# Performance work log

Hardware: AMD Instinct MI355X
Metric: run time of the kernel (lower is better)

## Reference

```python
import jax, jax.numpy as jnp
import numpy as np

B, C, T = 32, 256, 4096

def setup_inputs() -> dict:
    key = jax.random.key(0)
    k1, k2 = jax.random.split(key)
    x = jax.random.normal(k1, (B, C, T), dtype=jnp.float32)
    gamma = jax.random.normal(k2, (1,), dtype=jnp.float32)
    return {"x": x, "gamma": gamma}

def reference(x, gamma):
    # energy[b,i,j] = <x[b,i,:], x[b,j,:]>  -> (B, C, C)
    energy = jnp.einsum('bit,bjt->bij', x, x)
    # max-subtract trick: softmax over (rowmax - energy)
    energy_new = jnp.max(energy, axis=-1, keepdims=True) - energy
    attention = jax.nn.softmax(energy_new, axis=-1)
    # out[b,i,t] = sum_j attention[b,i,j] * x[b,j,t]
    out = jnp.einsum('bij,bjt->bit', attention, x)
    return gamma * out + x
```

## Files before the change

### kernel.cpp

```cpp
#include <hip/hip_runtime.h>
#include <hip/hip_bf16.h>

#define BATCH 32
#define CDIM  256
#define TDIM  4096

using short8  = __attribute__((ext_vector_type(8))) short;
using floatx4 = __attribute__((ext_vector_type(4))) float;
typedef unsigned short u16;

__device__ __forceinline__ unsigned f2bf(float f) {
  unsigned u = __float_as_uint(f);
  return (u + 0x7fffu + ((u >> 16) & 1u)) >> 16;
}
__device__ __forceinline__ unsigned cvt_pk_bf16(float a, float b) {
  return f2bf(a) | (f2bf(b) << 16);
}
__device__ __forceinline__ float bf_lo(unsigned u) { return __uint_as_float(u << 16); }
__device__ __forceinline__ float bf_hi(unsigned u) { return __uint_as_float(u & 0xffff0000u); }

__device__ __forceinline__ void glds16(const void* g, void* l) {
  __builtin_amdgcn_global_load_lds(
      (const __attribute__((address_space(1))) void*)g,
      (__attribute__((address_space(3))) void*)l, 16, 0, 0);
}

__global__ __launch_bounds__(256)
void split_t_kernel(const float* __restrict__ x, u16* __restrict__ hx,
                    u16* __restrict__ lx, u16* __restrict__ hxT) {
  __shared__ u16 ht[64][72];

  const int bx  = blockIdx.x;
  const int b   = bx >> 8;
  const int j0  = ((bx >> 6) & 3) << 6;
  const int t0  = (bx & 63) << 6;
  const int tid = threadIdx.x;
  const int jr  = tid >> 2;
  const int tc  = (tid & 3) << 4;

  const size_t xoff = ((size_t)b << 20) + (size_t)(j0 + jr) * TDIM + t0 + tc;
  const float4 a0 = ((const float4*)(x + xoff))[0];
  const float4 a1 = ((const float4*)(x + xoff))[1];
  const float4 a2 = ((const float4*)(x + xoff))[2];
  const float4 a3 = ((const float4*)(x + xoff))[3];
  const float4 aa[4] = {a0, a1, a2, a3};

  unsigned h[8], l[8];
#pragma unroll
  for (int u = 0; u < 4; ++u) {
    h[2 * u]     = cvt_pk_bf16(aa[u].x, aa[u].y);
    h[2 * u + 1] = cvt_pk_bf16(aa[u].z, aa[u].w);
    l[2 * u]     = cvt_pk_bf16(aa[u].x - bf_lo(h[2 * u]),     aa[u].y - bf_hi(h[2 * u]));
    l[2 * u + 1] = cvt_pk_bf16(aa[u].z - bf_lo(h[2 * u + 1]), aa[u].w - bf_hi(h[2 * u + 1]));
  }

  u16* ph = hx + xoff;
  *(uint4*)ph       = make_uint4(h[0], h[1], h[2], h[3]);
  *(uint4*)(ph + 8) = make_uint4(h[4], h[5], h[6], h[7]);
  u16* pl = lx + xoff;
  *(uint4*)pl       = make_uint4(l[0], l[1], l[2], l[3]);
  *(uint4*)(pl + 8) = make_uint4(l[4], l[5], l[6], l[7]);

#pragma unroll
  for (int u = 0; u < 16; ++u)
    ht[tc + u][jr] = (u16)((u & 1) ? (h[u >> 1] >> 16) : (h[u >> 1] & 0xffffu));
  __syncthreads();

  const int tr = tid >> 2;
  const int jc = (tid & 3) << 4;
  u16* pt = hxT + ((size_t)b << 20) + (size_t)(t0 + tr) * CDIM + j0 + jc;
  *(uint4*)pt       = *(const uint4*)&ht[tr][jc];
  *(uint4*)(pt + 8) = *(const uint4*)&ht[tr][jc + 8];
}

__global__ __launch_bounds__(256)
void split_kernel(const float* __restrict__ x, u16* __restrict__ hx,
                  u16* __restrict__ lx) {
  const unsigned gid0 = blockIdx.x * 256 + threadIdx.x;
#pragma unroll
  for (int it = 0; it < 8; ++it) {
    const size_t g8 = ((size_t)gid0 + (size_t)it * (2048u * 256u)) * 8;
    const float4 a = *(const float4*)(x + g8);
    const float4 c = *(const float4*)(x + g8 + 4);
    unsigned h0 = cvt_pk_bf16(a.x, a.y), h1 = cvt_pk_bf16(a.z, a.w);
    unsigned h2 = cvt_pk_bf16(c.x, c.y), h3 = cvt_pk_bf16(c.z, c.w);
    unsigned l0 = cvt_pk_bf16(a.x - bf_lo(h0), a.y - bf_hi(h0));
    unsigned l1 = cvt_pk_bf16(a.z - bf_lo(h1), a.w - bf_hi(h1));
    unsigned l2 = cvt_pk_bf16(c.x - bf_lo(h2), c.y - bf_hi(h2));
    unsigned l3 = cvt_pk_bf16(c.z - bf_lo(h3), c.w - bf_hi(h3));
    *(uint4*)(hx + g8) = make_uint4(h0, h1, h2, h3);
    *(uint4*)(lx + g8) = make_uint4(l0, l1, l2, l3);
  }
}

__global__ __launch_bounds__(512, 1)
void gram_gemm(const u16* __restrict__ hx, const u16* __restrict__ lx,
               float* __restrict__ S, float* __restrict__ E2) {
  __shared__ __align__(16) short lds[2 * 20480];

  const int tid = threadIdx.x;
  const int bx  = blockIdx.x;

  const int s8  = bx & 7;
  const int seq = bx >> 3;
  const int b   = s8 + ((seq >> 3) << 3);
  const int job = seq & 7;
  const int i0  = (job >> 2) << 7;
  const int j0  = (job & 3) << 6;

  const int lane = tid & 63;
  const int w    = tid >> 6;

  const int rsub = lane >> 3;
  const int gsw  = ((lane & 7) ^ rsub) << 3;
  const size_t xb = (size_t)b << 20;
  const u16* src[5];
  src[0] = hx + xb + (size_t)(i0 +      w * 8 + rsub) * TDIM + gsw;
  src[1] = hx + xb + (size_t)(i0 + 64 + w * 8 + rsub) * TDIM + gsw;
  src[2] = lx + xb + (size_t)(i0 +      w * 8 + rsub) * TDIM + gsw;
  src[3] = lx + xb + (size_t)(i0 + 64 + w * 8 + rsub) * TDIM + gsw;
  src[4] = hx + xb + (size_t)(j0 +      w * 8 + rsub) * TDIM + gsw;
  int dstoff[5];
#pragma unroll
  for (int s = 0; s < 5; ++s) dstoff[s] = (s * 8 + w) << 9;

  floatx4 acc1[2][2], acc2[2][2];
#pragma unroll
  for (int m = 0; m < 2; ++m)
#pragma unroll
    for (int n = 0; n < 2; ++n) {
      acc1[m][n] = {0.f, 0.f, 0.f, 0.f};
      acc2[m][n] = {0.f, 0.f, 0.f, 0.f};
    }

  const int wib = (w >> 1) << 5;
  const int wjb = (w & 1) << 5;
  const int fr  = lane & 15;
  const int q   = lane >> 4;
  const int f7  = fr & 7;

  const int g0 = ((q)     ^ f7) << 3;
  const int g1 = ((q + 4) ^ f7) << 3;
  const int a0 = (wib + fr) << 6;
  const int a1 = a0 + (16 << 6);
  const int b0 = (wjb + fr) << 6;
  const int b1 = b0 + (16 << 6);

#pragma unroll
  for (int s = 0; s < 5; ++s) glds16(src[s], lds + dstoff[s]);

  for (int ks = 0; ks < 64; ++ks) {
    const int bb = (ks & 1) * 20480;
    if (ks < 63) {
      const int nb = ((ks + 1) & 1) * 20480;
#pragma unroll
      for (int s = 0; s < 5; ++s)
        glds16(src[s] + ((ks + 1) << 6), lds + nb + dstoff[s]);
      asm volatile("s_waitcnt vmcnt(5)" ::: "memory");
    } else {
      asm volatile("s_waitcnt vmcnt(0)" ::: "memory");
    }
    __builtin_amdgcn_s_barrier();

    {
      short8 Ah0 = *(const short8*)&lds[bb + a0 + g0];
      short8 Ah1 = *(const short8*)&lds[bb + a1 + g0];
      short8 Al0 = *(const short8*)&lds[bb + 8192 + a0 + g0];
      short8 Al1 = *(const short8*)&lds[bb + 8192 + a1 + g0];
      short8 Bh0 = *(const short8*)&lds[bb + 16384 + b0 + g0];
      short8 Bh1 = *(const short8*)&lds[bb + 16384 + b1 + g0];
      acc1[0][0] = __builtin_amdgcn_mfma_f32_16x16x32_bf16(Ah0, Bh0, acc1[0][0], 0, 0, 0);
      acc1[0][1] = __builtin_amdgcn_mfma_f32_16x16x32_bf16(Ah0, Bh1, acc1[0][1], 0, 0, 0);
      acc1[1][0] = __builtin_amdgcn_mfma_f32_16x16x32_bf16(Ah1, Bh0, acc1[1][0], 0, 0, 0);
      acc1[1][1] = __builtin_amdgcn_mfma_f32_16x16x32_bf16(Ah1, Bh1, acc1[1][1], 0, 0, 0);
      acc2[0][0] = __builtin_amdgcn_mfma_f32_16x16x32_bf16(Al0, Bh0, acc2[0][0], 0, 0, 0);
      acc2[0][1] = __builtin_amdgcn_mfma_f32_16x16x32_bf16(Al0, Bh1, acc2[0][1], 0, 0, 0);
      acc2[1][0] = __builtin_amdgcn_mfma_f32_16x16x32_bf16(Al1, Bh0, acc2[1][0], 0, 0, 0);
      acc2[1][1] = __builtin_amdgcn_mfma_f32_16x16x32_bf16(Al1, Bh1, acc2[1][1], 0, 0, 0);
    }
    {
      short8 Ah0 = *(const short8*)&lds[bb + a0 + g1];
      short8 Ah1 = *(const short8*)&lds[bb + a1 + g1];
      short8 Al0 = *(const short8*)&lds[bb + 8192 + a0 + g1];
      short8 Al1 = *(const short8*)&lds[bb + 8192 + a1 + g1];
      short8 Bh0 = *(const short8*)&lds[bb + 16384 + b0 + g1];
      short8 Bh1 = *(const short8*)&lds[bb + 16384 + b1 + g1];
      acc1[0][0] = __builtin_amdgcn_mfma_f32_16x16x32_bf16(Ah0, Bh0, acc1[0][0], 0, 0, 0);
      acc1[0][1] = __builtin_amdgcn_mfma_f32_16x16x32_bf16(Ah0, Bh1, acc1[0][1], 0, 0, 0);
      acc1[1][0] = __builtin_amdgcn_mfma_f32_16x16x32_bf16(Ah1, Bh0, acc1[1][0], 0, 0, 0);
      acc1[1][1] = __builtin_amdgcn_mfma_f32_16x16x32_bf16(Ah1, Bh1, acc1[1][1], 0, 0, 0);
      acc2[0][0] = __builtin_amdgcn_mfma_f32_16x16x32_bf16(Al0, Bh0, acc2[0][0], 0, 0, 0);
      acc2[0][1] = __builtin_amdgcn_mfma_f32_16x16x32_bf16(Al0, Bh1, acc2[0][1], 0, 0, 0);
      acc2[1][0] = __builtin_amdgcn_mfma_f32_16x16x32_bf16(Al1, Bh0, acc2[1][0], 0, 0, 0);
      acc2[1][1] = __builtin_amdgcn_mfma_f32_16x16x32_bf16(Al1, Bh1, acc2[1][1], 0, 0, 0);
    }
    asm volatile("" ::: "memory");
    __builtin_amdgcn_s_barrier();
  }

#pragma unroll
  for (int m = 0; m < 2; ++m)
#pragma unroll
    for (int n = 0; n < 2; ++n) {
      const int gr = i0 + wib + 16 * m + 4 * q;
      const int gc = j0 + wjb + 16 * n + fr;
      size_t base = (((size_t)b * CDIM + gr) << 8) + gc;
#pragma unroll
      for (int r = 0; r < 4; ++r) {
        S[base + ((size_t)r << 8)]  = acc1[m][n][r] + acc2[m][n][r];
        E2[base + ((size_t)r << 8)] = acc2[m][n][r];
      }
    }
}

__global__ __launch_bounds__(512, 1)
void gram_fused(const float* __restrict__ x,
                float* __restrict__ S, float* __restrict__ E2) {
  __shared__ __align__(16) short hI[128 * 64];
  __shared__ __align__(16) short lI[128 * 64];
  __shared__ __align__(16) short hJ[64 * 64];

  const int tid = threadIdx.x;
  const int bx  = blockIdx.x;
  const int s   = bx & 7;
  const int seq = bx >> 3;
  const int b   = s + ((seq >> 3) << 3);
  const int job = seq & 7;
  const int i0  = (job >> 2) << 7;
  const int j0  = (job & 3) << 6;

  const float* xb = x + ((size_t)b << 20);

  const bool isJ   = tid >= 256;
  const int  irow  = tid >> 1;
  const int  ihalf = tid & 1;
  const int  jrow  = (tid & 255) >> 2;
  const int  jq    = tid & 3;

  const float* pS = isJ
      ? xb + (size_t)(j0 + jrow) * TDIM + (jq << 4)
      : xb + (size_t)(i0 + irow) * TDIM + (ihalf << 5);

  floatx4 acc1[2][2], acc2[2][2];
#pragma unroll
  for (int m = 0; m < 2; ++m)
#pragma unroll
    for (int n = 0; n < 2; ++n) {
      acc1[m][n] = {0.f, 0.f, 0.f, 0.f};
      acc2[m][n] = {0.f, 0.f, 0.f, 0.f};
    }

  const int lane = tid & 63;
  const int w    = tid >> 6;
  const int wib  = (w >> 1) << 5;
  const int wjb  = (w & 1) << 5;
  const int fr   = lane & 15;
  const int q    = lane >> 4;
  const int f7   = fr & 7;

  const int g0 = ((q)     ^ f7) << 3;
  const int g1 = ((q + 4) ^ f7) << 3;
  const int a0 = (wib + fr) << 6;
  const int a1 = a0 + (16 << 6);
  const int b0 = (wjb + fr) << 6;
  const int b1 = b0 + (16 << 6);

  float4 r0, r1, r2, r3, r4, r5, r6, r7;
  r0 = ((const float4*)pS)[0]; r1 = ((const float4*)pS)[1];
  r2 = ((const float4*)pS)[2]; r3 = ((const float4*)pS)[3];
  if (!isJ) {
    r4 = ((const float4*)pS)[4]; r5 = ((const float4*)pS)[5];
    r6 = ((const float4*)pS)[6]; r7 = ((const float4*)pS)[7];
  }

  for (int ks = 0; ks < TDIM / 64; ++ks) {
    unsigned h0 = cvt_pk_bf16(r0.x, r0.y), h1 = cvt_pk_bf16(r0.z, r0.w);
    unsigned h2 = cvt_pk_bf16(r1.x, r1.y), h3 = cvt_pk_bf16(r1.z, r1.w);
    unsigned h4 = cvt_pk_bf16(r2.x, r2.y), h5 = cvt_pk_bf16(r2.z, r2.w);
    unsigned h6 = cvt_pk_bf16(r3.x, r3.y), h7 = cvt_pk_bf16(r3.z, r3.w);
    unsigned h8, h9, hA, hB, hC, hD, hE, hF;
    unsigned l0, l1, l2, l3, l4, l5, l6, l7, l8, l9, lA, lB, lC, lD, lE, lF;
    if (!isJ) {
      h8 = cvt_pk_bf16(r4.x, r4.y); h9 = cvt_pk_bf16(r4.z, r4.w);
      hA = cvt_pk_bf16(r5.x, r5.y); hB = cvt_pk_bf16(r5.z, r5.w);
      hC = cvt_pk_bf16(r6.x, r6.y); hD = cvt_pk_bf16(r6.z, r6.w);
      hE = cvt_pk_bf16(r7.x, r7.y); hF = cvt_pk_bf16(r7.z, r7.w);
      l0 = cvt_pk_bf16(r0.x - bf_lo(h0), r0.y - bf_hi(h0));
      l1 = cvt_pk_bf16(r0.z - bf_lo(h1), r0.w - bf_hi(h1));
      l2 = cvt_pk_bf16(r1.x - bf_lo(h2), r1.y - bf_hi(h2));
      l3 = cvt_pk_bf16(r1.z - bf_lo(h3), r1.w - bf_hi(h3));
      l4 = cvt_pk_bf16(r2.x - bf_lo(h4), r2.y - bf_hi(h4));
      l5 = cvt_pk_bf16(r2.z - bf_lo(h5), r2.w - bf_hi(h5));
      l6 = cvt_pk_bf16(r3.x - bf_lo(h6), r3.w - bf_hi(h6));
      l6 = cvt_pk_bf16(r3.x - bf_lo(h6), r3.y - bf_hi(h6));
      l7 = cvt_pk_bf16(r3.z - bf_lo(h7), r3.w - bf_hi(h7));
      l8 = cvt_pk_bf16(r4.x - bf_lo(h8), r4.y - bf_hi(h8));
      l9 = cvt_pk_bf16(r4.z - bf_lo(h9), r4.w - bf_hi(h9));
      lA = cvt_pk_bf16(r5.x - bf_lo(hA), r5.y - bf_hi(hA));
      lB = cvt_pk_bf16(r5.z - bf_lo(hB), r5.w - bf_hi(hB));
      lC = cvt_pk_bf16(r6.x - bf_lo(hC), r6.y - bf_hi(hC));
      lD = cvt_pk_bf16(r6.z - bf_lo(hD), r6.w - bf_hi(hD));
      lE = cvt_pk_bf16(r7.x - bf_lo(hE), r7.y - bf_hi(hE));
      lF = cvt_pk_bf16(r7.z - bf_lo(hF), r7.w - bf_hi(hF));
    }

    __syncthreads();
    if (!isJ) {
      const int rb = irow << 6;
      const int s7 = irow & 7;
      const int gb = ihalf << 2;
      *(uint4*)&hI[rb + (((gb + 0) ^ s7) << 3)] = make_uint4(h0, h1, h2, h3);
      *(uint4*)&hI[rb + (((gb + 1) ^ s7) << 3)] = make_uint4(h4, h5, h6, h7);
      *(uint4*)&hI[rb + (((gb + 2) ^ s7) << 3)] = make_uint4(h8, h9, hA, hB);
      *(uint4*)&hI[rb + (((gb + 3) ^ s7) << 3)] = make_uint4(hC, hD, hE, hF);
      *(uint4*)&lI[rb + (((gb + 0) ^ s7) << 3)] = make_uint4(l0, l1, l2, l3);
      *(uint4*)&lI[rb + (((gb + 1) ^ s7) << 3)] = make_uint4(l4, l5, l6, l7);
      *(uint4*)&lI[rb + (((gb + 2) ^ s7) << 3)] = make_uint4(l8, l9, lA, lB);
      *(uint4*)&lI[rb + (((gb + 3) ^ s7) << 3)] = make_uint4(lC, lD, lE, lF);
    } else {
      const int rb = jrow << 6;
      const int s7 = jrow & 7;
      const int gb = jq << 1;
      *(uint4*)&hJ[rb + (((gb + 0) ^ s7) << 3)] = make_uint4(h0, h1, h2, h3);
      *(uint4*)&hJ[rb + (((gb + 1) ^ s7) << 3)] = make_uint4(h4, h5, h6, h7);
    }
    __syncthreads();

    if (ks < TDIM / 64 - 1) {
      pS += 64;
      r0 = ((const float4*)pS)[0]; r1 = ((const float4*)pS)[1];
      r2 = ((const float4*)pS)[2]; r3 = ((const float4*)pS)[3];
      if (!isJ) {
        r4 = ((const float4*)pS)[4]; r5 = ((const float4*)pS)[5];
        r6 = ((const float4*)pS)[6]; r7 = ((const float4*)pS)[7];
      }
    }

    {
      short8 Ah0 = *(const short8*)&hI[a0 + g0];
      short8 Ah1 = *(const short8*)&hI[a1 + g0];
      short8 Al0 = *(const short8*)&lI[a0 + g0];
      short8 Al1 = *(const short8*)&lI[a1 + g0];
      short8 Bh0 = *(const short8*)&hJ[b0 + g0];
      short8 Bh1 = *(const short8*)&hJ[b1 + g0];
      acc1[0][0] = __builtin_amdgcn_mfma_f32_16x16x32_bf16(Ah0, Bh0, acc1[0][0], 0, 0, 0);
      acc1[0][1] = __builtin_amdgcn_mfma_f32_16x16x32_bf16(Ah0, Bh1, acc1[0][1], 0, 0, 0);
      acc1[1][0] = __builtin_amdgcn_mfma_f32_16x16x32_bf16(Ah1, Bh0, acc1[1][0], 0, 0, 0);
      acc1[1][1] = __builtin_amdgcn_mfma_f32_16x16x32_bf16(Ah1, Bh1, acc1[1][1], 0, 0, 0);
      acc2[0][0] = __builtin_amdgcn_mfma_f32_16x16x32_bf16(Al0, Bh0, acc2[0][0], 0, 0, 0);
      acc2[0][1] = __builtin_amdgcn_mfma_f32_16x16x32_bf16(Al0, Bh1, acc2[0][1], 0, 0, 0);
      acc2[1][0] = __builtin_amdgcn_mfma_f32_16x16x32_bf16(Al1, Bh0, acc2[1][0], 0, 0, 0);
      acc2[1][1] = __builtin_amdgcn_mfma_f32_16x16x32_bf16(Al1, Bh1, acc2[1][1], 0, 0, 0);
    }
    {
      short8 Ah0 = *(const short8*)&hI[a0 + g1];
      short8 Ah1 = *(const short8*)&hI[a1 + g1];
      short8 Al0 = *(const short8*)&lI[a0 + g1];
      short8 Al1 = *(const short8*)&lI[a1 + g1];
      short8 Bh0 = *(const short8*)&hJ[b0 + g1];
      short8 Bh1 = *(const short8*)&hJ[b1 + g1];
      acc1[0][0] = __builtin_amdgcn_mfma_f32_16x16x32_bf16(Ah0, Bh0, acc1[0][0], 0, 0, 0);
      acc1[0][1] = __builtin_amdgcn_mfma_f32_16x16x32_bf16(Ah0, Bh1, acc1[0][1], 0, 0, 0);
      acc1[1][0] = __builtin_amdgcn_mfma_f32_16x16x32_bf16(Ah1, Bh0, acc1[1][0], 0, 0, 0);
      acc1[1][1] = __builtin_amdgcn_mfma_f32_16x16x32_bf16(Ah1, Bh1, acc1[1][1], 0, 0, 0);
      acc2[0][0] = __builtin_amdgcn_mfma_f32_16x16x32_bf16(Al0, Bh0, acc2[0][0], 0, 0, 0);
      acc2[0][1] = __builtin_amdgcn_mfma_f32_16x16x32_bf16(Al0, Bh1, acc2[0][1], 0, 0, 0);
      acc2[1][0] = __builtin_amdgcn_mfma_f32_16x16x32_bf16(Al1, Bh0, acc2[1][0], 0, 0, 0);
      acc2[1][1] = __builtin_amdgcn_mfma_f32_16x16x32_bf16(Al1, Bh1, acc2[1][1], 0, 0, 0);
    }
  }

#pragma unroll
  for (int m = 0; m < 2; ++m)
#pragma unroll
    for (int n = 0; n < 2; ++n) {
      const int gr = i0 + wib + 16 * m + 4 * q;
      const int gc = j0 + wjb + 16 * n + fr;
      size_t base = (((size_t)b * CDIM + gr) << 8) + gc;
#pragma unroll
      for (int r = 0; r < 4; ++r) {
        S[base + ((size_t)r << 8)]  = acc1[m][n][r] + acc2[m][n][r];
        E2[base + ((size_t)r << 8)] = acc2[m][n][r];
      }
    }
}

__global__ __launch_bounds__(256)
void softmax_kernel(const float* __restrict__ S, const float* __restrict__ E2,
                    __hip_bfloat16* __restrict__ att) {
  __shared__ float SR[32][264];
  __shared__ float ST[256][33];

  const int tid = threadIdx.x;
  const int b   = blockIdx.x >> 3;
  const int i0  = (blockIdx.x & 7) << 5;
  const size_t base = (size_t)b << 16;

  {
    const int r  = tid >> 3;
    const int c0 = (tid & 7) << 5;
    const float* p1 = S + base + ((size_t)(i0 + r) << 8) + c0;
#pragma unroll
    for (int u = 0; u < 32; u += 4)
      *(float4*)&SR[r][c0 + u] = *(const float4*)(p1 + u);
  }
  {
    const int c  = tid & 31;
    const int j0 = (tid >> 5) << 5;
    const float* p = E2 + base + i0 + c;
#pragma unroll
    for (int jj = 0; jj < 32; ++jj)
      ST[j0 + jj][c] = p[(size_t)(j0 + jj) << 8];
  }
  __syncthreads();

  const int r  = tid >> 3;
  const int t7 = tid & 7;
  float z[32];
  float m = -3.4e38f;
#pragma unroll
  for (int k = 0; k < 32; ++k) {
    const int j = t7 + (k << 3);
    const float e = SR[r][j] + ST[j][r];
    z[k] = -e;
    m = fmaxf(m, z[k]);
  }
  m = fmaxf(m, __shfl_xor(m, 1, 64));
  m = fmaxf(m, __shfl_xor(m, 2, 64));
  m = fmaxf(m, __shfl_xor(m, 4, 64));
  float ssum = 0.f;
#pragma unroll
  for (int k = 0; k < 32; ++k) { z[k] = expf(z[k] - m); ssum += z[k]; }
  ssum += __shfl_xor(ssum, 1, 64);
  ssum += __shfl_xor(ssum, 2, 64);
  ssum += __shfl_xor(ssum, 4, 64);
  const float inv = 1.f / ssum;

  u16* arow = (u16*)att + base + ((size_t)(i0 + r) << 8);
#pragma unroll
  for (int k = 0; k < 32; ++k) {
    const int j = t7 + (k << 3);
    arow[j] = (u16)f2bf(z[k] * inv);
  }
}

__global__ __launch_bounds__(512, 1)
void pv_kernel(const float* __restrict__ x, const u16* __restrict__ hxT,
               const __hip_bfloat16* __restrict__ att,
               const float* __restrict__ gamma, float* __restrict__ out) {
  __shared__ __align__(16) short As[128 * 256];
  __shared__ __align__(16) short Bs[128 * 256];

  const int tid = threadIdx.x;
  const int bx  = blockIdx.x;
  const int b   = bx >> 6;
  const int i0  = ((bx >> 5) & 1) << 7;
  const int t0  = (bx & 31) << 7;

  const u16* asrc = (const u16*)att + ((size_t)b << 16) + ((size_t)i0 << 8);
  const u16* bsrc = hxT + ((size_t)b << 20) + ((size_t)t0 << 8);

  const int lane = tid & 63;
  const int w    = tid >> 6;

  const int rh = lane >> 5;
  const int gd = lane & 31;
#pragma unroll
  for (int s = 0; s < 8; ++s) {
    const int c  = (s << 3) + w;
    const int r  = (c << 1) + rh;
    const int gs = gd ^ (r & 7);
    glds16(asrc + ((size_t)r << 8) + (gs << 3), As + (c << 9));
  }
#pragma unroll
  for (int s = 0; s < 8; ++s) {
    const int c  = (s << 3) + w;
    const int r  = (c << 1) + rh;
    const int gs = gd ^ (r & 7);
    glds16(bsrc + ((size_t)r << 8) + (gs << 3), Bs + (c << 9));
  }

  floatx4 acc[4][2];
#pragma unroll
  for (int m = 0; m < 4; ++m)
#pragma unroll
    for (int n = 0; n < 2; ++n) acc[m][n] = {0.f, 0.f, 0.f, 0.f};

  const int wm = (w >> 2) << 6;
  const int wn = (w & 3) << 5;
  const int fr = lane & 15;
  const int q  = lane >> 4;

  __syncthreads();

#pragma unroll
  for (int ks = 0; ks < 8; ++ks) {
    short8 Af[4], Bf[2];
#pragma unroll
    for (int m = 0; m < 4; ++m) {
      const int r = wm + 16 * m + fr;
      const int g = ((ks << 2) + q) ^ (r & 7);
      Af[m] = *(const short8*)(As + r * 256 + (g << 3));
    }
#pragma unroll
    for (int n = 0; n < 2; ++n) {
      const int r = wn + 16 * n + fr;
      const int g = ((ks << 2) + q) ^ (r & 7);
      Bf[n] = *(const short8*)(Bs + r * 256 + (g << 3));
    }
#pragma unroll
    for (int m = 0; m < 4; ++m)
#pragma unroll
      for (int n = 0; n < 2; ++n)
        acc[m][n] = __builtin_amdgcn_mfma_f32_16x16x32_bf16(Af[m], Bf[n], acc[m][n], 0, 0, 0);
  }

  const float g = gamma[0];
#pragma unroll
  for (int m = 0; m < 4; ++m)
#pragma unroll
    for (int n = 0; n < 2; ++n) {
      const int gr = i0 + wm + 16 * m + 4 * q;
      const int gc = t0 + wn + 16 * n + fr;
      size_t base = ((size_t)b << 20) + (size_t)gr * TDIM + gc;
#pragma unroll
      for (int r = 0; r < 4; ++r) {
        size_t idx = base + (size_t)r * TDIM;
        out[idx] = g * acc[m][n][r] + x[idx];
      }
    }
}

__global__ __launch_bounds__(256, 1)
void pv_fused(const float* __restrict__ x, const __hip_bfloat16* __restrict__ att,
              const float* __restrict__ gamma, float* __restrict__ out) {
  __shared__ __align__(16) short As[128 * 256];
  __shared__ __align__(16) short Bs[128 * 256];

  const int tid = threadIdx.x;
  const int bx  = blockIdx.x;
  const int b   = bx >> 6;
  const int i0  = ((bx >> 5) & 1) << 7;
  const int t0  = (bx & 31) << 7;

  const float* xb = x + ((size_t)b << 20) + t0;
  const u16* attb = (const u16*)att + ((size_t)b << 16) + ((size_t)i0 << 8);

  {
    uint4 areg[16];
#pragma unroll
    for (int c = 0; c < 16; ++c) {
      const int p = (c << 8) + tid;
      const int r = p >> 5;
      const int g = (p & 31) ^ (r & 7);
      areg[c] = *(const uint4*)(attb + (r << 8) + (g << 3));
    }
#pragma unroll
    for (int c = 0; c < 16; ++c) {
      const int p = (c << 8) + tid;
      *(uint4*)((char*)As + ((size_t)p << 4)) = areg[c];
    }
  }
  {
    const int tQ = tid & 31;
    const int jg = tid >> 5;
#pragma unroll
    for (int j8 = 0; j8 < 4; ++j8) {
      floatx4 v[8];
#pragma unroll
      for (int u = 0; u < 8; ++u) {
        const int j = (jg << 5) + (j8 << 3) + u;
        v[u] = *(const floatx4*)(xb + (size_t)j * TDIM + (tQ << 2));
      }
#pragma unroll
      for (int tt = 0; tt < 4; ++tt) {
        uint4 wv = make_uint4(cvt_pk_bf16(v[0][tt], v[1][tt]),
                              cvt_pk_bf16(v[2][tt], v[3][tt]),
                              cvt_pk_bf16(v[4][tt], v[5][tt]),
                              cvt_pk_bf16(v[6][tt], v[7][tt]));
        const int row = (tQ << 2) + tt;
        const int gx  = ((jg << 2) + j8) ^ (row & 7);
        *(uint4*)((char*)Bs + (size_t)row * 512 + ((size_t)gx << 4)) = wv;
      }
    }
  }

  floatx4 acc[4][4];
#pragma unroll
  for (int m = 0; m < 4; ++m)
#pragma unroll
    for (int n = 0; n < 4; ++n) acc[m][n] = {0.f, 0.f, 0.f, 0.f};

  const int lane = tid & 63;
  const int w    = tid >> 6;
  const int wm   = (w >> 1) << 6;
  const int wn   = (w & 1) << 6;
  const int fr   = lane & 15;
  const int q    = lane >> 4;

  __syncthreads();

#pragma unroll
  for (int ks = 0; ks < 8; ++ks) {
    short8 Af[4], Bf[4];
#pragma unroll
    for (int m = 0; m < 4; ++m) {
      const int r = wm + 16 * m + fr;
      const int g = ((ks << 2) + q) ^ (r & 7);
      Af[m] = *(const short8*)((char*)As + (size_t)r * 512 + ((size_t)g << 4));
    }
#pragma unroll
    for (int n = 0; n < 4; ++n) {
      const int r = wn + 16 * n + fr;
      const int g = ((ks << 2) + q) ^ (r & 7);
      Bf[n] = *(const short8*)((char*)Bs + (size_t)r * 512 + ((size_t)g << 4));
    }
#pragma unroll
    for (int m = 0; m < 4; ++m)
#pragma unroll
      for (int n = 0; n < 4; ++n)
        acc[m][n] = __builtin_amdgcn_mfma_f32_16x16x32_bf16(Af[m], Bf[n], acc[m][n], 0, 0, 0);
  }

  const float g = gamma[0];
#pragma unroll
  for (int m = 0; m < 4; ++m)
#pragma unroll
    for (int n = 0; n < 4; ++n) {
      const int gr = i0 + wm + 16 * m + 4 * q;
      const int gc = t0 + wn + 16 * n + fr;
      size_t base = ((size_t)b << 20) + (size_t)gr * TDIM + gc;
#pragma unroll
      for (int r = 0; r < 4; ++r) {
        size_t idx = base + (size_t)r * TDIM;
        out[idx] = g * acc[m][n][r] + x[idx];
      }
    }
}

extern "C" void kernel_launch(void* const* d_in, const int* in_sizes, int n_in,
                              void* d_out, int out_size, void* d_ws, size_t ws_size,
                              hipStream_t stream) {
  (void)in_sizes; (void)n_in; (void)out_size;
  const float* x     = (const float*)d_in[0];
  const float* gamma = (const float*)d_in[1];
  float* out = (float*)d_out;

  const size_t MB = 1024 * 1024;
  const size_t EN = (size_t)BATCH * CDIM * CDIM;
  const size_t XN = (size_t)BATCH * CDIM * TDIM;
  float* S  = (float*)d_ws;
  float* E2 = S + EN;
  __hip_bfloat16* att = (__hip_bfloat16*)(E2 + EN);
  u16* hx  = (u16*)((char*)d_ws + 20 * MB);
  u16* lx  = hx + XN;
  u16* hxT = lx + XN;
  const size_t need_full = 20 * MB + 3 * XN * sizeof(u16);
  const size_t need_mid  = 20 * MB + 2 * XN * sizeof(u16);

  if (ws_size >= need_full) {
    split_t_kernel<<<dim3(8192), dim3(256), 0, stream>>>(x, hx, lx, hxT);
    gram_gemm<<<dim3(256), dim3(512), 0, stream>>>(hx, lx, S, E2);
    softmax_kernel<<<dim3(BATCH * 8), dim3(256), 0, stream>>>(S, E2, att);
    pv_kernel<<<dim3(2048), dim3(512), 0, stream>>>(x, hxT, att, gamma, out);
  } else if (ws_size >= need_mid) {
    split_kernel<<<dim3(2048), dim3(256), 0, stream>>>(x, hx, lx);
    gram_gemm<<<dim3(256), dim3(512), 0, stream>>>(hx, lx, S, E2);
    softmax_kernel<<<dim3(BATCH * 8), dim3(256), 0, stream>>>(S, E2, att);
    pv_fused<<<dim3(2048), dim3(256), 0, stream>>>(x, att, gamma, out);
  } else {
    gram_fused<<<dim3(256), dim3(512), 0, stream>>>(x, S, E2);
    softmax_kernel<<<dim3(BATCH * 8), dim3(256), 0, stream>>>(S, E2, att);
    pv_fused<<<dim3(2048), dim3(256), 0, stream>>>(x, att, gamma, out);
  }
}
```

Baseline: 403.9 us.

## Enlarge split/transpose tiles and halve gram GEMM blocks for more parallelism

New measurement: 428.7 us. 6.2% more time.

```diff
diff --git a/kernel.cpp b/kernel.cpp
--- a/kernel.cpp
+++ b/kernel.cpp
@@ -26,51 +26,68 @@
 }
 
 __global__ __launch_bounds__(256)
-void split_t_kernel(const float* __restrict__ x, u16* __restrict__ hx,
-                    u16* __restrict__ lx, u16* __restrict__ hxT) {
-  __shared__ u16 ht[64][72];
+void split_t2_kernel(const float* __restrict__ x, u16* __restrict__ hx,
+                     u16* __restrict__ lx, u16* __restrict__ hxT) {
+  __shared__ u16 hs[128 * 128];
 
   const int bx  = blockIdx.x;
-  const int b   = bx >> 8;
-  const int j0  = ((bx >> 6) & 3) << 6;
-  const int t0  = (bx & 63) << 6;
+  const int b   = bx >> 6;
+  const int j0  = ((bx >> 5) & 1) << 7;
+  const int t0  = (bx & 31) << 7;
   const int tid = threadIdx.x;
-  const int jr  = tid >> 2;
-  const int tc  = (tid & 3) << 4;
-
-  const size_t xoff = ((size_t)b << 20) + (size_t)(j0 + jr) * TDIM + t0 + tc;
-  const float4 a0 = ((const float4*)(x + xoff))[0];
-  const float4 a1 = ((const float4*)(x + xoff))[1];
-  const float4 a2 = ((const float4*)(x + xoff))[2];
-  const float4 a3 = ((const float4*)(x + xoff))[3];
-  const float4 aa[4] = {a0, a1, a2, a3};
-
-  unsigned h[8], l[8];
-#pragma unroll
-  for (int u = 0; u < 4; ++u) {
-    h[2 * u]     = cvt_pk_bf16(aa[u].x, aa[u].y);
-    h[2 * u + 1] = cvt_pk_bf16(aa[u].z, aa[u].w);
-    l[2 * u]     = cvt_pk_bf16(aa[u].x - bf_lo(h[2 * u]),     aa[u].y - bf_hi(h[2 * u]));
-    l[2 * u + 1] = cvt_pk_bf16(aa[u].z - bf_lo(h[2 * u + 1]), aa[u].w - bf_hi(h[2 * u + 1]));
+  const int jr   = tid >> 1;
+  const int half = tid & 1;
+  const int tl0  = half << 6;
+
+  const size_t xoff = ((size_t)b << 20) + (size_t)(j0 + jr) * TDIM + t0 + tl0;
+
+  float4 a[16];
+#pragma unroll
+  for (int u = 0; u < 16; ++u) a[u] = ((const float4*)(x + xoff))[u];
+
+  unsigned h[32], l[32];
+#pragma unroll
+  for (int u = 0; u < 16; ++u) {
+    h[2 * u]     = cvt_pk_bf16(a[u].x, a[u].y);
+    h[2 * u + 1] = cvt_pk_bf16(a[u].z, a[u].w);
+    l[2 * u]     = cvt_pk_bf16(a[u].x - bf_lo(h[2 * u]),     a[u].y - bf_hi(h[2 * u]));
+    l[2 * u + 1] = cvt_pk_bf16(a[u].z - bf_lo(h[2 * u + 1]), a[u].w - bf_hi(h[2 * u + 1]));
   }
 
   u16* ph = hx + xoff;
-  *(uint4*)ph       = make_uint4(h[0], h[1], h[2], h[3]);
-  *(uint4*)(ph + 8) = make_uint4(h[4], h[5], h[6], h[7]);
   u16* pl = lx + xoff;
-  *(uint4*)pl       = make_uint4(l[0], l[1], l[2], l[3]);
-  *(uint4*)(pl + 8) = make_uint4(l[4], l[5], l[6], l[7]);
-
-#pragma unroll
-  for (int u = 0; u < 16; ++u)
-    ht[tc + u][jr] = (u16)((u & 1) ? (h[u >> 1] >> 16) : (h[u >> 1] & 0xffffu));
+#pragma unroll
+  for (int u = 0; u < 8; ++u) {
+    ((uint4*)ph)[u] = make_uint4(h[4 * u], h[4 * u + 1], h[4 * u + 2], h[4 * u + 3]);
+    ((uint4*)pl)[u] = make_uint4(l[4 * u], l[4 * u + 1], l[4 * u + 2], l[4 * u + 3]);
+  }
+
+#pragma unroll
+  for (int g = 0; g < 8; ++g) {
+    const int gg = tl0 / 8 + g;
+    const int gs = gg ^ (jr & 15);
+    *(uint4*)&hs[jr * 128 + (gs << 3)] =
+        make_uint4(h[4 * g], h[4 * g + 1], h[4 * g + 2], h[4 * g + 3]);
+  }
   __syncthreads();
 
-  const int tr = tid >> 2;
-  const int jc = (tid & 3) << 4;
-  u16* pt = hxT + ((size_t)b << 20) + (size_t)(t0 + tr) * CDIM + j0 + jc;
-  *(uint4*)pt       = *(const uint4*)&ht[tr][jc];
-  *(uint4*)(pt + 8) = *(const uint4*)&ht[tr][jc + 8];
+  const int tr = tid >> 1;
+  const int jh = half << 6;
+  const int gt = tr >> 3;
+  const int t7 = tr & 7;
+  unsigned o[32];
+#pragma unroll
+  for (int p = 0; p < 32; ++p) {
+    const int j1 = jh + 2 * p;
+    const int j2 = j1 + 1;
+    const unsigned lo = hs[j1 * 128 + ((gt ^ (j1 & 15)) << 3) + t7];
+    const unsigned hi = hs[j2 * 128 + ((gt ^ (j2 & 15)) << 3) + t7];
+    o[p] = lo | (hi << 16);
+  }
+  u16* pt = hxT + ((size_t)b << 20) + (size_t)(t0 + tr) * CDIM + j0 + jh;
+#pragma unroll
+  for (int u = 0; u < 8; ++u)
+    ((uint4*)pt)[u] = make_uint4(o[4 * u], o[4 * u + 1], o[4 * u + 2], o[4 * u + 3]);
 }
 
 __global__ __launch_bounds__(256)
@@ -93,19 +110,19 @@
   }
 }
 
-__global__ __launch_bounds__(512, 1)
+__global__ __launch_bounds__(256, 2)
 void gram_gemm(const u16* __restrict__ hx, const u16* __restrict__ lx,
                float* __restrict__ S, float* __restrict__ E2) {
-  __shared__ __align__(16) short lds[2 * 20480];
+  __shared__ __align__(16) short lds[2 * 12288];
 
   const int tid = threadIdx.x;
   const int bx  = blockIdx.x;
 
   const int s8  = bx & 7;
   const int seq = bx >> 3;
-  const int b   = s8 + ((seq >> 3) << 3);
-  const int job = seq & 7;
-  const int i0  = (job >> 2) << 7;
+  const int b   = s8 + ((seq >> 4) << 3);
+  const int job = seq & 15;
+  const int i0  = (job >> 2) << 6;
   const int j0  = (job & 3) << 6;
 
   const int lane = tid & 63;
@@ -114,15 +131,19 @@
   const int rsub = lane >> 3;
   const int gsw  = ((lane & 7) ^ rsub) << 3;
   const size_t xb = (size_t)b << 20;
-  const u16* src[5];
-  src[0] = hx + xb + (size_t)(i0 +      w * 8 + rsub) * TDIM + gsw;
-  src[1] = hx + xb + (size_t)(i0 + 64 + w * 8 + rsub) * TDIM + gsw;
-  src[2] = lx + xb + (size_t)(i0 +      w * 8 + rsub) * TDIM + gsw;
-  src[3] = lx + xb + (size_t)(i0 + 64 + w * 8 + rsub) * TDIM + gsw;
-  src[4] = hx + xb + (size_t)(j0 +      w * 8 + rsub) * TDIM + gsw;
-  int dstoff[5];
-#pragma unroll
-  for (int s = 0; s < 5; ++s) dstoff[s] = (s * 8 + w) << 9;
+  const u16* src[6];
+  int dstoff[6];
+#pragma unroll
+  for (int s = 0; s < 6; ++s) {
+    const int c = (s << 2) + w;
+    const u16* base;
+    int row;
+    if (c < 8)       { base = hx; row = i0 + (c << 3) + rsub; }
+    else if (c < 16) { base = lx; row = i0 + ((c - 8) << 3) + rsub; }
+    else             { base = hx; row = j0 + ((c - 16) << 3) + rsub; }
+    src[s]    = base + xb + (size_t)row * TDIM + gsw;
+    dstoff[s] = c << 9;
+  }
 
   floatx4 acc1[2][2], acc2[2][2];
 #pragma unroll
@@ -147,16 +168,16 @@
   const int b1 = b0 + (16 << 6);
 
 #pragma unroll
-  for (int s = 0; s < 5; ++s) glds16(src[s], lds + dstoff[s]);
+  for (int s = 0; s < 6; ++s) glds16(src[s], lds + dstoff[s]);
 
   for (int ks = 0; ks < 64; ++ks) {
-    const int bb = (ks & 1) * 20480;
+    const int bb = (ks & 1) * 12288;
     if (ks < 63) {
-      const int nb = ((ks + 1) & 1) * 20480;
-#pragma unroll
-      for (int s = 0; s < 5; ++s)
+      const int nb = ((ks + 1) & 1) * 12288;
+#pragma unroll
+      for (int s = 0; s < 6; ++s)
         glds16(src[s] + ((ks + 1) << 6), lds + nb + dstoff[s]);
-      asm volatile("s_waitcnt vmcnt(5)" ::: "memory");
+      asm volatile("s_waitcnt vmcnt(6)" ::: "memory");
     } else {
       asm volatile("s_waitcnt vmcnt(0)" ::: "memory");
     }
@@ -165,10 +186,10 @@
     {
       short8 Ah0 = *(const short8*)&lds[bb + a0 + g0];
       short8 Ah1 = *(const short8*)&lds[bb + a1 + g0];
-      short8 Al0 = *(const short8*)&lds[bb + 8192 + a0 + g0];
-      short8 Al1 = *(const short8*)&lds[bb + 8192 + a1 + g0];
-      short8 Bh0 = *(const short8*)&lds[bb + 16384 + b0 + g0];
-      short8 Bh1 = *(const short8*)&lds[bb + 16384 + b1 + g0];
+      short8 Al0 = *(const short8*)&lds[bb + 4096 + a0 + g0];
+      short8 Al1 = *(const short8*)&lds[bb + 4096 + a1 + g0];
+      short8 Bh0 = *(const short8*)&lds[bb + 8192 + b0 + g0];
+      short8 Bh1 = *(const short8*)&lds[bb + 8192 + b1 + g0];
       acc1[0][0] = __builtin_amdgcn_mfma_f32_16x16x32_bf16(Ah0, Bh0, acc1[0][0], 0, 0, 0);
       acc1[0][1] = __builtin_amdgcn_mfma_f32_16x16x32_bf16(Ah0, Bh1, acc1[0][1], 0, 0, 0);
       acc1[1][0] = __builtin_amdgcn_mfma_f32_16x16x32_bf16(Ah1, Bh0, acc1[1][0], 0, 0, 0);
@@ -181,10 +202,10 @@
     {
       short8 Ah0 = *(const short8*)&lds[bb + a0 + g1];
       short8 Ah1 = *(const short8*)&lds[bb + a1 + g1];
-      short8 Al0 = *(const short8*)&lds[bb + 8192 + a0 + g1];
-      short8 Al1 = *(const short8*)&lds[bb + 8192 + a1 + g1];
-      short8 Bh0 = *(const short8*)&lds[bb + 16384 + b0 + g1];
-      short8 Bh1 = *(const short8*)&lds[bb + 16384 + b1 + g1];
+      short8 Al0 = *(const short8*)&lds[bb + 4096 + a0 + g1];
+      short8 Al1 = *(const short8*)&lds[bb + 4096 + a1 + g1];
+      short8 Bh0 = *(const short8*)&lds[bb + 8192 + b0 + g1];
+      short8 Bh1 = *(const short8*)&lds[bb + 8192 + b1 + g1];
       acc1[0][0] = __builtin_amdgcn_mfma_f32_16x16x32_bf16(Ah0, Bh0, acc1[0][0], 0, 0, 0);
       acc1[0][1] = __builtin_amdgcn_mfma_f32_16x16x32_bf16(Ah0, Bh1, acc1[0][1], 0, 0, 0);
       acc1[1][0] = __builtin_amdgcn_mfma_f32_16x16x32_bf16(Ah1, Bh0, acc1[1][0], 0, 0, 0);
@@ -291,7 +312,6 @@
       l3 = cvt_pk_bf16(r1.z - bf_lo(h3), r1.w - bf_hi(h3));
       l4 = cvt_pk_bf16(r2.x - bf_lo(h4), r2.y - bf_hi(h4));
       l5 = cvt_pk_bf16(r2.z - bf_lo(h5), r2.w - bf_hi(h5));
-      l6 = cvt_pk_bf16(r3.x - bf_lo(h6), r3.w - bf_hi(h6));
       l6 = cvt_pk_bf16(r3.x - bf_lo(h6), r3.y - bf_hi(h6));
       l7 = cvt_pk_bf16(r3.z - bf_lo(h7), r3.w - bf_hi(h7));
       l8 = cvt_pk_bf16(r4.x - bf_lo(h8), r4.y - bf_hi(h8));
@@ -659,13 +679,13 @@
   const size_t need_mid  = 20 * MB + 2 * XN * sizeof(u16);
 
   if (ws_size >= need_full) {
-    split_t_kernel<<<dim3(8192), dim3(256), 0, stream>>>(x, hx, lx, hxT);
-    gram_gemm<<<dim3(256), dim3(512), 0, stream>>>(hx, lx, S, E2);
+    split_t2_kernel<<<dim3(2048), dim3(256), 0, stream>>>(x, hx, lx, hxT);
+    gram_gemm<<<dim3(512), dim3(256), 0, stream>>>(hx, lx, S, E2);
     softmax_kernel<<<dim3(BATCH * 8), dim3(256), 0, stream>>>(S, E2, att);
     pv_kernel<<<dim3(2048), dim3(512), 0, stream>>>(x, hxT, att, gamma, out);
   } else if (ws_size >= need_mid) {
     split_kernel<<<dim3(2048), dim3(256), 0, stream>>>(x, hx, lx);
-    gram_gemm<<<dim3(256), dim3(512), 0, stream>>>(hx, lx, S, E2);
+    gram_gemm<<<dim3(512), dim3(256), 0, stream>>>(hx, lx, S, E2);
     softmax_kernel<<<dim3(BATCH * 8), dim3(256), 0, stream>>>(S, E2, att);
     pv_fused<<<dim3(2048), dim3(256), 0, stream>>>(x, att, gamma, out);
   } else {
```
